# Kernel optimization log

Hardware: AMD Instinct MI355X
Metric: run time of the kernel (lower is better)

The kernel has to match this reference:

```python
import jax, jax.numpy as jnp
import numpy as np

# Grid / layout constants (match init_kwargs)
NX, NY = 2048, 2048
XL, YL = 0.0, 0.0
HX = 1.0 / NX  # bin_size_x
HY = 1.0 / NY  # bin_size_y
NUM_NODES = 1_000_000
NUM_MOVABLE = 900_000


def compute_velocity_field(phi, hx, hy):
    """v = -grad(phi) via central differences, one-sided at boundaries.
    phi: [nx, ny] -> (vx, vy) each [nx, ny]."""
    vx = jnp.concatenate([
        -(phi[1:2, :] - phi[0:1, :]) / hx,          # forward diff at x=0
        -(phi[2:, :] - phi[:-2, :]) / (2.0 * hx),   # central in interior
        -(phi[-1:, :] - phi[-2:-1, :]) / hx,        # backward diff at x=nx-1
    ], axis=0)
    vy = jnp.concatenate([
        -(phi[:, 1:2] - phi[:, 0:1]) / hy,
        -(phi[:, 2:] - phi[:, :-2]) / (2.0 * hy),
        -(phi[:, -1:] - phi[:, -2:-1]) / hy,
    ], axis=1)
    return vx, vy


def setup_inputs() -> dict:
    key = jax.random.key(0)
    k1, k2 = jax.random.split(key)
    # Node positions in [0,1)x[0,1): x coords then y coords.
    pos = jax.random.uniform(k1, (2 * NUM_NODES,), dtype=jnp.float32)
    # Solved transport potential on the bin grid (stand-in for multigrid output).
    potential_field = jax.random.normal(k2, (NX, NY), dtype=jnp.float32)
    return {"pos": pos, "potential_field": potential_field}


def reference(pos, potential_field):
    # Forward of FlowBasedDensityPotentialFunction (post-solve part):
    # velocity = -grad(phi); energy = 0.5 * sum(|v|^2).
    vx, vy = compute_velocity_field(potential_field, HX, HY)
    energy = 0.5 * (jnp.sum(vx * vx) + jnp.sum(vy * vy))
    return energy
```

## Files before the change

kernel.cpp:

```cpp
#include <hip/hip_runtime.h>

#define NXG 2048
#define NYG 2048
__device__ __forceinline__ float inv_h()  { return 2048.0f; }
__device__ __forceinline__ float inv_2h() { return 1024.0f; }

#define BLOCK 256
#define GRID  1024

__global__ __launch_bounds__(BLOCK) void
energy_partial_kernel(const float* __restrict__ phi, float* __restrict__ partial) {
    const int totalChunks = (NXG / 2) * (NYG / 4);
    float acc = 0.0f;

    for (int c = blockIdx.x * blockDim.x + threadIdx.x;
         c < totalChunks;
         c += gridDim.x * blockDim.x) {
        const int p  = c >> 9;
        const int j4 = (c & 511) << 2;
        const int i0 = 2 * p;
        const int i1 = i0 + 1;

        const int rm = (p > 0)            ? i0 - 1 : 0;
        const int rp = (p < NXG / 2 - 1)  ? i1 + 1 : NXG - 1;
        const float sx0 = (i0 == 0)       ? inv_h() : inv_2h();
        const float sx1 = (i1 == NXG - 1) ? inv_h() : inv_2h();

        const float* rowm = phi + (size_t)rm * NYG;
        const float* row0 = phi + (size_t)i0 * NYG;
        const float* row1 = phi + (size_t)i1 * NYG;
        const float* rowp = phi + (size_t)rp * NYG;

        const float4 a = *(const float4*)(rowm + j4);
        const float4 b = *(const float4*)(row0 + j4);
        const float4 g = *(const float4*)(row1 + j4);
        const float4 d = *(const float4*)(rowp + j4);

        const float vxa0 = (g.x - a.x) * sx0, vxa1 = (g.y - a.y) * sx0;
        const float vxa2 = (g.z - a.z) * sx0, vxa3 = (g.w - a.w) * sx0;
        const float vxb0 = (d.x - b.x) * sx1, vxb1 = (d.y - b.y) * sx1;
        const float vxb2 = (d.z - b.z) * sx1, vxb3 = (d.w - b.w) * sx1;

        float vya0, vya3, vyb0, vyb3;
        if (j4 == 0) {
            vya0 = (b.y - b.x) * inv_h();
            vyb0 = (g.y - g.x) * inv_h();
        } else {
            vya0 = (b.y - row0[j4 - 1]) * inv_2h();
            vyb0 = (g.y - row1[j4 - 1]) * inv_2h();
        }
        const float vya1 = (b.z - b.x) * inv_2h();
        const float vya2 = (b.w - b.y) * inv_2h();
        const float vyb1 = (g.z - g.x) * inv_2h();
        const float vyb2 = (g.w - g.y) * inv_2h();
        if (j4 + 4 == NYG) {
            vya3 = (b.w - b.z) * inv_h();
            vyb3 = (g.w - g.z) * inv_h();
        } else {
            vya3 = (row0[j4 + 4] - b.z) * inv_2h();
            vyb3 = (row1[j4 + 4] - g.z) * inv_2h();
        }

        acc += vxa0 * vxa0 + vxa1 * vxa1 + vxa2 * vxa2 + vxa3 * vxa3
             + vxb0 * vxb0 + vxb1 * vxb1 + vxb2 * vxb2 + vxb3 * vxb3
             + vya0 * vya0 + vya1 * vya1 + vya2 * vya2 + vya3 * vya3
             + vyb0 * vyb0 + vyb1 * vyb1 + vyb2 * vyb2 + vyb3 * vyb3;
    }

    #pragma unroll
    for (int off = 32; off > 0; off >>= 1)
        acc += __shfl_down(acc, off, 64);

    __shared__ float smem[BLOCK / 64];
    const int lane = threadIdx.x & 63;
    const int wave = threadIdx.x >> 6;
    if (lane == 0) smem[wave] = acc;
    __syncthreads();
    if (threadIdx.x == 0) {
        float s = 0.0f;
        #pragma unroll
        for (int w = 0; w < BLOCK / 64; ++w) s += smem[w];
        partial[blockIdx.x] = s;
    }
}

__global__ __launch_bounds__(BLOCK) void
energy_finalize_kernel(const float* __restrict__ partial, float* __restrict__ out) {
    float acc = 0.0f;
    for (int idx = threadIdx.x; idx < GRID; idx += BLOCK)
        acc += partial[idx];

    #pragma unroll
    for (int off = 32; off > 0; off >>= 1)
        acc += __shfl_down(acc, off, 64);

    __shared__ float smem[BLOCK / 64];
    const int lane = threadIdx.x & 63;
    const int wave = threadIdx.x >> 6;
    if (lane == 0) smem[wave] = acc;
    __syncthreads();
    if (threadIdx.x == 0) {
        float s = 0.0f;
        #pragma unroll
        for (int w = 0; w < BLOCK / 64; ++w) s += smem[w];
        out[0] = 0.5f * s;
    }
}

extern "C" void kernel_launch(void* const* d_in, const int* in_sizes, int n_in,
                              void* d_out, int out_size, void* d_ws, size_t ws_size,
                              hipStream_t stream) {
    const float* phi = (const float*)d_in[1];
    float* out = (float*)d_out;
    float* partial = (float*)d_ws;

    energy_partial_kernel<<<GRID, BLOCK, 0, stream>>>(phi, partial);
    energy_finalize_kernel<<<1, BLOCK, 0, stream>>>(partial, out);
}
```

Before: 73.09 us.

## Process four rows per thread and remap blocks across XCDs

Each thread now handles a 4-row by 4-column tile in a single pass with no grid-stride loop. It loads 6 rows instead of 4 rows per 2 output rows, which cuts redundant row reads for the x-stencil. Block indices are remapped so consecutive tiles land on the same XCD, to improve L2 sharing of halo rows. The mapping relies on GRID*BLOCK exactly covering the domain, and accumulation switches to fmaf.

```diff
diff --git a/kernel.cpp b/kernel.cpp
--- a/kernel.cpp
+++ b/kernel.cpp
@@ -7,64 +7,79 @@
 
 #define BLOCK 256
 #define GRID  1024
+#define NXCD  8
 
 __global__ __launch_bounds__(BLOCK) void
 energy_partial_kernel(const float* __restrict__ phi, float* __restrict__ partial) {
-    const int totalChunks = (NXG / 2) * (NYG / 4);
+    const int slot = blockIdx.x;
+    const int wg   = (slot & (NXCD - 1)) * (GRID / NXCD) + (slot >> 3);
+    const int c    = wg * BLOCK + threadIdx.x;
+
+    const int g  = c >> 9;
+    const int j4 = (c & 511) << 2;
+    const int r0 = 4 * g;
+
+    const int rm = (g > 0)   ? r0 - 1 : 0;
+    const int rp = (g < 511) ? r0 + 4 : NXG - 1;
+    const float sx0 = (r0 == 0)  ? inv_h() : inv_2h();
+    const float sx3 = (g == 511) ? inv_h() : inv_2h();
+
+    const float* rowm = phi + (size_t)rm * NYG;
+    const float* row0 = phi + (size_t)r0 * NYG;
+    const float* row1 = row0 + NYG;
+    const float* row2 = row1 + NYG;
+    const float* row3 = row2 + NYG;
+    const float* rowp = phi + (size_t)rp * NYG;
+
+    const float4 a  = *(const float4*)(rowm + j4);
+    const float4 b0 = *(const float4*)(row0 + j4);
+    const float4 b1 = *(const float4*)(row1 + j4);
+    const float4 b2 = *(const float4*)(row2 + j4);
+    const float4 b3 = *(const float4*)(row3 + j4);
+    const float4 d  = *(const float4*)(rowp + j4);
+
     float acc = 0.0f;
 
-    for (int c = blockIdx.x * blockDim.x + threadIdx.x;
-         c < totalChunks;
-         c += gridDim.x * blockDim.x) {
-        const int p  = c >> 9;
-        const int j4 = (c & 511) << 2;
-        const int i0 = 2 * p;
-        const int i1 = i0 + 1;
+    {
+        float v;
+        v = (b1.x - a.x) * sx0;      acc = fmaf(v, v, acc);
+        v = (b1.y - a.y) * sx0;      acc = fmaf(v, v, acc);
+        v = (b1.z - a.z) * sx0;      acc = fmaf(v, v, acc);
+        v = (b1.w - a.w) * sx0;      acc = fmaf(v, v, acc);
+        v = (b2.x - b0.x) * inv_2h(); acc = fmaf(v, v, acc);
+        v = (b2.y - b0.y) * inv_2h(); acc = fmaf(v, v, acc);
+        v = (b2.z - b0.z) * inv_2h(); acc = fmaf(v, v, acc);
+        v = (b2.w - b0.w) * inv_2h(); acc = fmaf(v, v, acc);
+        v = (b3.x - b1.x) * inv_2h(); acc = fmaf(v, v, acc);
+        v = (b3.y - b1.y) * inv_2h(); acc = fmaf(v, v, acc);
+        v = (b3.z - b1.z) * inv_2h(); acc = fmaf(v, v, acc);
+        v = (b3.w - b1.w) * inv_2h(); acc = fmaf(v, v, acc);
+        v = (d.x - b2.x) * sx3;      acc = fmaf(v, v, acc);
+        v = (d.y - b2.y) * sx3;      acc = fmaf(v, v, acc);
+        v = (d.z - b2.z) * sx3;      acc = fmaf(v, v, acc);
+        v = (d.w - b2.w) * sx3;      acc = fmaf(v, v, acc);
+    }
 
-        const int rm = (p > 0)            ? i0 - 1 : 0;
-        const int rp = (p < NXG / 2 - 1)  ? i1 + 1 : NXG - 1;
-        const float sx0 = (i0 == 0)       ? inv_h() : inv_2h();
-        const float sx1 = (i1 == NXG - 1) ? inv_h() : inv_2h();
-
-        const float* rowm = phi + (size_t)rm * NYG;
-        const float* row0 = phi + (size_t)i0 * NYG;
-        const float* row1 = phi + (size_t)i1 * NYG;
-        const float* rowp = phi + (size_t)rp * NYG;
-
-        const float4 a = *(const float4*)(rowm + j4);
-        const float4 b = *(const float4*)(row0 + j4);
-        const float4 g = *(const float4*)(row1 + j4);
-        const float4 d = *(const float4*)(rowp + j4);
-
-        const float vxa0 = (g.x - a.x) * sx0, vxa1 = (g.y - a.y) * sx0;
-        const float vxa2 = (g.z - a.z) * sx0, vxa3 = (g.w - a.w) * sx0;
-        const float vxb0 = (d.x - b.x) * sx1, vxb1 = (d.y - b.y) * sx1;
-        const float vxb2 = (d.z - b.z) * sx1, vxb3 = (d.w - b.w) * sx1;
-
-        float vya0, vya3, vyb0, vyb3;
+    const float4 rows[4] = { b0, b1, b2, b3 };
+    const float* rptr[4] = { row0, row1, row2, row3 };
+    #pragma unroll
+    for (int r = 0; r < 4; ++r) {
+        const float4 v4 = rows[r];
+        float v;
         if (j4 == 0) {
-            vya0 = (b.y - b.x) * inv_h();
-            vyb0 = (g.y - g.x) * inv_h();
+            v = (v4.y - v4.x) * inv_h();
         } else {
-            vya0 = (b.y - row0[j4 - 1]) * inv_2h();
-            vyb0 = (g.y - row1[j4 - 1]) * inv_2h();
+            v = (v4.y - rptr[r][j4 - 1]) * inv_2h();
         }
-        const float vya1 = (b.z - b.x) * inv_2h();
-        const float vya2 = (b.w - b.y) * inv_2h();
-        const float vyb1 = (g.z - g.x) * inv_2h();
-        const float vyb2 = (g.w - g.y) * inv_2h();
+        acc = fmaf(v, v, acc);
+        v = (v4.z - v4.x) * inv_2h(); acc = fmaf(v, v, acc);
+        v = (v4.w - v4.y) * inv_2h(); acc = fmaf(v, v, acc);
         if (j4 + 4 == NYG) {
-            vya3 = (b.w - b.z) * inv_h();
-            vyb3 = (g.w - g.z) * inv_h();
+            v = (v4.w - v4.z) * inv_h();
         } else {
-            vya3 = (row0[j4 + 4] - b.z) * inv_2h();
-            vyb3 = (row1[j4 + 4] - g.z) * inv_2h();
+            v = (rptr[r][j4 + 4] - v4.z) * inv_2h();
         }
-
-        acc += vxa0 * vxa0 + vxa1 * vxa1 + vxa2 * vxa2 + vxa3 * vxa3
-             + vxb0 * vxb0 + vxb1 * vxb1 + vxb2 * vxb2 + vxb3 * vxb3
-             + vya0 * vya0 + vya1 * vya1 + vya2 * vya2 + vya3 * vya3
-             + vyb0 * vyb0 + vyb1 * vyb1 + vyb2 * vyb2 + vyb3 * vyb3;
+        acc = fmaf(v, v, acc);
     }
 
     #pragma unroll
```

New measurement: 72.84 us. Within noise of the previous version (-0.3%).
